# Kernel tuning notes

Measured on AMD Instinct MI355X. Metric: run time of the kernel, lower is better.

The kernel has to match this reference:

```python
import jax, jax.numpy as jnp
import numpy as np

D_MODEL = 1024
N_HEADS = 16
D_HEAD = D_MODEL // N_HEADS
B, S = 2, 2048


def setup_inputs() -> dict:
    key = jax.random.key(0)
    ks = jax.random.split(key, 14)
    std = 0.02
    inp = {
        "query": jax.random.normal(ks[0], (B, S, D_MODEL), dtype=jnp.float32),
        "key": jax.random.normal(ks[1], (B, S, D_MODEL), dtype=jnp.float32),
        "value": jax.random.normal(ks[2], (B, S, D_MODEL), dtype=jnp.float32),
        "mask": jax.random.randint(ks[3], (B, 1, S, S), 0, 2, dtype=jnp.int32),
        "position_bias": jax.random.normal(ks[4], (1, N_HEADS, S, S), dtype=jnp.float32),
        "w_q": jax.random.normal(ks[5], (D_MODEL, D_MODEL), dtype=jnp.float32) * std,
        "b_q": jnp.zeros((D_MODEL,), dtype=jnp.float32),
        "w_k": jax.random.normal(ks[6], (D_MODEL, D_MODEL), dtype=jnp.float32) * std,
        "b_k": jnp.zeros((D_MODEL,), dtype=jnp.float32),
        "w_v": jax.random.normal(ks[7], (D_MODEL, D_MODEL), dtype=jnp.float32) * std,
        "b_v": jnp.zeros((D_MODEL,), dtype=jnp.float32),
        "w_o": jax.random.normal(ks[8], (D_MODEL, D_MODEL), dtype=jnp.float32) * std,
        "b_o": jnp.zeros((D_MODEL,), dtype=jnp.float32),
    }
    return inp


def reference(query, key, value, mask, position_bias,
              w_q, b_q, w_k, b_k, w_v, b_v, w_o, b_o):
    b = query.shape[0]
    # projections: torch Linear computes x @ W^T + b
    def proj(x, w, bias):
        y = x @ w.T + bias                       # [b, s, D]
        return y.reshape(b, -1, N_HEADS, D_HEAD).transpose(0, 2, 1, 3)  # [b, h, s, d]

    Q = proj(query, w_q, b_q)
    K = proj(key, w_k, b_k)
    V = proj(value, w_v, b_v)

    scale = 1.0 / jnp.sqrt(jnp.asarray(D_HEAD, dtype=Q.dtype))
    scores = jnp.einsum("bhqd,bhkd->bhqk", Q, K) * scale
    scores = scores + position_bias
    scores = jnp.where(mask == 0, jnp.asarray(-1e9, dtype=scores.dtype), scores)
    attn = jax.nn.softmax(scores, axis=-1)       # dropout is identity at eval
    ctx = jnp.einsum("bhqk,bhkd->bhqd", attn, V)  # [b, h, s, d]
    ctx = ctx.transpose(0, 2, 1, 3).reshape(b, -1, N_HEADS * D_HEAD)
    return ctx @ w_o.T + b_o
```

## Files before the change

### kernel.cpp

```cpp
#include <hip/hip_runtime.h>
#include <hip/hip_bf16.h>

#define S_LEN 2048
#define DM 1024
#define NH 16
#define DH 64
#define MTOK 4096

typedef __attribute__((ext_vector_type(8))) __bf16 bf16x8;
typedef __attribute__((ext_vector_type(4))) float f32x4;
typedef unsigned short u16;
typedef unsigned long long u64;

__device__ __forceinline__ u16 f2bf(float f) {
  union { float f; unsigned u; } a; a.f = f;
  unsigned u = a.u;
  u += 0x7fffu + ((u >> 16) & 1u);
  return (u16)(u >> 16);
}

__device__ __forceinline__ bf16x8 ld_bf8(const u16* p) {
  return *reinterpret_cast<const bf16x8*>(p);
}

__device__ __forceinline__ float f4get(const float4& v, int r) {
  switch (r & 3) { case 0: return v.x; case 1: return v.y; case 2: return v.z; default: return v.w; }
}

__global__ void k_convert_all(
    const float* __restrict__ w_q, const float* __restrict__ w_k,
    const float* __restrict__ w_v, const float* __restrict__ w_o,
    const float* __restrict__ q, const float* __restrict__ k, const float* __restrict__ v,
    u16* __restrict__ dwq, u16* __restrict__ dwk, u16* __restrict__ dwv,
    u16* __restrict__ dwo, u16* __restrict__ dq, u16* __restrict__ dk, u16* __restrict__ dv,
    int n4w, int n4x) {
  const int z = blockIdx.y;
  const float* s; u16* d; int n4;
  switch (z) {
    case 0: s = w_q; d = dwq; n4 = n4w; break;
    case 1: s = w_k; d = dwk; n4 = n4w; break;
    case 2: s = w_v; d = dwv; n4 = n4w; break;
    case 3: s = w_o; d = dwo; n4 = n4w; break;
    case 4: s = q;   d = dq;  n4 = n4x; break;
    case 5: s = k;   d = dk;  n4 = n4x; break;
    default: s = v;  d = dv;  n4 = n4x; break;
  }
  int i = blockIdx.x * blockDim.x + threadIdx.x;
  const int stride = gridDim.x * blockDim.x;
  for (; i < n4; i += stride) {
    float4 vv = reinterpret_cast<const float4*>(s)[i];
    ushort4 o;
    o.x = f2bf(vv.x); o.y = f2bf(vv.y); o.z = f2bf(vv.z); o.w = f2bf(vv.w);
    reinterpret_cast<ushort4*>(d)[i] = o;
  }
}

__global__ void k_maskpack(const int* __restrict__ m, u64* __restrict__ o, int n) {
  int i = blockIdx.x * blockDim.x + threadIdx.x;
  int stride = gridDim.x * blockDim.x;
  for (; i < n; i += stride) {
    u64 bal = __ballot(m[i] != 0);
    if ((i & 63) == 0) o[i >> 6] = bal;
  }
}

__global__ __launch_bounds__(256) void k_gemm_qkv(
    const u16* __restrict__ xq, const u16* __restrict__ xk, const u16* __restrict__ xv,
    const u16* __restrict__ wq, const u16* __restrict__ wk, const u16* __restrict__ wv,
    const float* __restrict__ bq, const float* __restrict__ bk, const float* __restrict__ bvb,
    u16* __restrict__ Qd, u16* __restrict__ Kd, u16* __restrict__ Vd) {
  constexpr int K = DM;
  __shared__ u16 As[128 * 32];
  __shared__ u16 Bs[128 * 32];
  const int z = blockIdx.z;
  const u16* A  = z == 0 ? xq : z == 1 ? xk : xv;
  const u16* Bw = z == 0 ? wq : z == 1 ? wk : wv;
  const float* bias = z == 0 ? bq : z == 1 ? bk : bvb;
  const int tid = threadIdx.x;
  const int lane = tid & 63;
  const int wid = tid >> 6;
  const int wm = wid >> 1, wn = wid & 1;
  const int bm = blockIdx.x * 128;
  const int bn = blockIdx.y * 128;
  const int r0 = tid >> 2;
  const int c0 = (tid & 3) * 8;
  const int fr = lane & 15;
  const int fk = (lane >> 4) * 8;

  f32x4 acc[4][4] = {};

  const u16* ga = A + (size_t)(bm + r0) * K + c0;
  const u16* gb = Bw + (size_t)(bn + r0) * K + c0;

  for (int kt = 0; kt < K; kt += 32) {
    __syncthreads();
    __builtin_amdgcn_global_load_lds(
        (const __attribute__((address_space(1))) void*)(ga + kt),
        (__attribute__((address_space(3))) void*)(&As[r0 * 32 + c0]), 16, 0, 0);
    __builtin_amdgcn_global_load_lds(
        (const __attribute__((address_space(1))) void*)(ga + (size_t)64 * K + kt),
        (__attribute__((address_space(3))) void*)(&As[(r0 + 64) * 32 + c0]), 16, 0, 0);
    __builtin_amdgcn_global_load_lds(
        (const __attribute__((address_space(1))) void*)(gb + kt),
        (__attribute__((address_space(3))) void*)(&Bs[r0 * 32 + c0]), 16, 0, 0);
    __builtin_amdgcn_global_load_lds(
        (const __attribute__((address_space(1))) void*)(gb + (size_t)64 * K + kt),
        (__attribute__((address_space(3))) void*)(&Bs[(r0 + 64) * 32 + c0]), 16, 0, 0);
    __syncthreads();
    bf16x8 af[4], bfr[4];
#pragma unroll
    for (int m = 0; m < 4; ++m) af[m] = ld_bf8(&As[(wm * 64 + m * 16 + fr) * 32 + fk]);
#pragma unroll
    for (int n = 0; n < 4; ++n) bfr[n] = ld_bf8(&Bs[(wn * 64 + n * 16 + fr) * 32 + fk]);
#pragma unroll
    for (int m = 0; m < 4; ++m)
#pragma unroll
      for (int n = 0; n < 4; ++n)
        acc[m][n] = __builtin_amdgcn_mfma_f32_16x16x32_bf16(af[m], bfr[n], acc[m][n], 0, 0, 0);
  }

  const int cr = (lane >> 4) * 4;
  const int cc = lane & 15;
#pragma unroll
  for (int m = 0; m < 4; ++m) {
#pragma unroll
    for (int n = 0; n < 4; ++n) {
      const int colg = bn + wn * 64 + n * 16 + cc;
      const float bv = bias[colg];
      const int rbase = bm + wm * 64 + m * 16 + cr;
      const int hh = colg >> 6, d = colg & 63;
      if (z < 2) {
        u16* o = z == 0 ? Qd : Kd;
#pragma unroll
        for (int r = 0; r < 4; ++r) {
          const int tok = rbase + r;
          const int b = tok >> 11, s = tok & 2047;
          o[(((size_t)(b * NH + hh) * S_LEN) + s) * DH + d] = f2bf(acc[m][n][r] + bv);
        }
      } else {
        const int tok = rbase;
        const int b = tok >> 11, s = tok & 2047;
        ushort4 pk;
        pk.x = f2bf(acc[m][n][0] + bv);
        pk.y = f2bf(acc[m][n][1] + bv);
        pk.z = f2bf(acc[m][n][2] + bv);
        pk.w = f2bf(acc[m][n][3] + bv);
        *reinterpret_cast<ushort4*>(&Vd[(((size_t)(b * NH + hh) * DH) + d) * S_LEN + s]) = pk;
      }
    }
  }
}

__global__ __launch_bounds__(256) void k_gemm_out(
    const u16* __restrict__ A, const u16* __restrict__ Bw,
    const float* __restrict__ bias, float* __restrict__ dst) {
  constexpr int K = DM;
  __shared__ u16 As[128 * 32];
  __shared__ u16 Bs[128 * 32];
  const int tid = threadIdx.x;
  const int lane = tid & 63;
  const int wid = tid >> 6;
  const int wm = wid >> 1, wn = wid & 1;
  const int bm = blockIdx.x * 128;
  const int bn = blockIdx.y * 128;
  const int r0 = tid >> 2;
  const int c0 = (tid & 3) * 8;
  const int fr = lane & 15;
  const int fk = (lane >> 4) * 8;

  f32x4 acc[4][4] = {};

  const u16* ga = A + (size_t)(bm + r0) * K + c0;
  const u16* gb = Bw + (size_t)(bn + r0) * K + c0;

  for (int kt = 0; kt < K; kt += 32) {
    __syncthreads();
    __builtin_amdgcn_global_load_lds(
        (const __attribute__((address_space(1))) void*)(ga + kt),
        (__attribute__((address_space(3))) void*)(&As[r0 * 32 + c0]), 16, 0, 0);
    __builtin_amdgcn_global_load_lds(
        (const __attribute__((address_space(1))) void*)(ga + (size_t)64 * K + kt),
        (__attribute__((address_space(3))) void*)(&As[(r0 + 64) * 32 + c0]), 16, 0, 0);
    __builtin_amdgcn_global_load_lds(
        (const __attribute__((address_space(1))) void*)(gb + kt),
        (__attribute__((address_space(3))) void*)(&Bs[r0 * 32 + c0]), 16, 0, 0);
    __builtin_amdgcn_global_load_lds(
        (const __attribute__((address_space(1))) void*)(gb + (size_t)64 * K + kt),
        (__attribute__((address_space(3))) void*)(&Bs[(r0 + 64) * 32 + c0]), 16, 0, 0);
    __syncthreads();
    bf16x8 af[4], bfr[4];
#pragma unroll
    for (int m = 0; m < 4; ++m) af[m] = ld_bf8(&As[(wm * 64 + m * 16 + fr) * 32 + fk]);
#pragma unroll
    for (int n = 0; n < 4; ++n) bfr[n] = ld_bf8(&Bs[(wn * 64 + n * 16 + fr) * 32 + fk]);
#pragma unroll
    for (int m = 0; m < 4; ++m)
#pragma unroll
      for (int n = 0; n < 4; ++n)
        acc[m][n] = __builtin_amdgcn_mfma_f32_16x16x32_bf16(af[m], bfr[n], acc[m][n], 0, 0, 0);
  }

  const int cr = (lane >> 4) * 4;
  const int cc = lane & 15;
#pragma unroll
  for (int m = 0; m < 4; ++m) {
#pragma unroll
    for (int n = 0; n < 4; ++n) {
      const int colg = bn + wn * 64 + n * 16 + cc;
      const float bv = bias[colg];
      const int rbase = bm + wm * 64 + m * 16 + cr;
#pragma unroll
      for (int r = 0; r < 4; ++r)
        dst[(size_t)(rbase + r) * DM + colg] = acc[m][n][r] + bv;
    }
  }
}

__global__ __launch_bounds__(256, 4) void k_attn(
    const u16* __restrict__ Qb, const u16* __restrict__ Kb, const u16* __restrict__ Vt,
    const float* __restrict__ bias, const u64* __restrict__ mpk,
    u16* __restrict__ ctx) {
  __shared__ u16 lds[2][2][4096];
  const int tid = threadIdx.x;
  const int lane = tid & 63;
  const int w = tid >> 6;
  const int b = blockIdx.z;
  const int h = blockIdx.y;
  const int q0 = blockIdx.x * 64 + w * 16;
  const int lq = lane & 15;
  const int lg = lane >> 4;

  const float* bp = bias + (size_t)h * S_LEN * S_LEN;
  const u16* Kp = Kb + (size_t)(b * NH + h) * S_LEN * DH;
  const u16* Vp = Vt + (size_t)(b * NH + h) * DH * S_LEN;

  bf16x8 qf[2];
  f32x4 cacc[4] = {};
  float l_run = 0.f;
  {
    const u16* Qp = Qb + (size_t)(b * NH + h) * S_LEN * DH;
    qf[0] = ld_bf8(&Qp[(size_t)(q0 + lq) * DH + lg * 8]);
    qf[1] = ld_bf8(&Qp[(size_t)(q0 + lq) * DH + 32 + lg * 8]);
  }

#define STAGE(ktv, cb) {                                                          \
    _Pragma("unroll") for (int i = 0; i < 2; ++i) {                               \
      const int el = (i * 256 + tid) * 8;                                         \
      const int rr = el >> 6;                                                     \
      const int ce = ((tid & 7) * 8) ^ ((rr & 7) << 3);                           \
      const u16* ksrc = Kp + (size_t)((ktv) + rr) * DH + ce;                      \
      const u16* vsrc = Vp + (size_t)rr * S_LEN + (ktv) + ce;                     \
      __builtin_amdgcn_global_load_lds(                                           \
          (const __attribute__((address_space(1))) void*)ksrc,                    \
          (__attribute__((address_space(3))) void*)&lds[cb][0][el], 16, 0, 0);    \
      __builtin_amdgcn_global_load_lds(                                           \
          (const __attribute__((address_space(1))) void*)vsrc,                    \
          (__attribute__((address_space(3))) void*)&lds[cb][1][el], 16, 0, 0);    \
    } }

#define SWZ(row, col) ((row) * 64 + (((((col) >> 3) ^ ((row) & 7)) << 3) | ((col) & 7)))

#define LOADB(ktv, tv) {                                                          \
    bv0 = *reinterpret_cast<const float4*>(                                       \
        &bp[(size_t)(q0 + lq) * S_LEN + (ktv) + 0 * 16 + lg * 4]);                \
    bv1 = *reinterpret_cast<const float4*>(                                       \
        &bp[(size_t)(q0 + lq) * S_LEN + (ktv) + 1 * 16 + lg * 4]);                \
    bv2 = *reinterpret_cast<const float4*>(                                       \
        &bp[(size_t)(q0 + lq) * S_LEN + (ktv) + 2 * 16 + lg * 4]);                \
    bv3 = *reinterpret_cast<const float4*>(                                       \
        &bp[(size_t)(q0 + lq) * S_LEN + (ktv) + 3 * 16 + lg * 4]);                \
    mw = mpk[((size_t)(b * S_LEN + q0 + lq)) * 32 + (tv)]; }

  float4 bv0, bv1, bv2, bv3;
  u64 mw;
  STAGE(0, 0);
  LOADB(0, 0);
  int c = 0;
  for (int t = 0; t < S_LEN / 64; ++t) {
    __syncthreads();
    if (t + 1 < S_LEN / 64) STAGE(t * 64 + 64, c ^ 1);

    f32x4 sc[4];
    __builtin_amdgcn_s_setprio(1);
#pragma unroll
    for (int nb = 0; nb < 4; ++nb) {
      bf16x8 kf0 = ld_bf8(&lds[c][0][SWZ(nb * 16 + lq, lg * 8)]);
      bf16x8 kf1 = ld_bf8(&lds[c][0][SWZ(nb * 16 + lq, 32 + lg * 8)]);
      f32x4 z = {};
      z = __builtin_amdgcn_mfma_f32_16x16x32_bf16(kf0, qf[0], z, 0, 0, 0);
      sc[nb] = __builtin_amdgcn_mfma_f32_16x16x32_bf16(kf1, qf[1], z, 0, 0, 0);
    }
    __builtin_amdgcn_s_setprio(0);

#pragma unroll
    for (int r = 0; r < 4; ++r) {
      const int sh = lg * 4 + r;
      sc[0][r] = ((mw >> (sh))      & 1) ? sc[0][r] * 0.125f + f4get(bv0, r) : -1e9f;
      sc[1][r] = ((mw >> (16 + sh)) & 1) ? sc[1][r] * 0.125f + f4get(bv1, r) : -1e9f;
      sc[2][r] = ((mw >> (32 + sh)) & 1) ? sc[2][r] * 0.125f + f4get(bv2, r) : -1e9f;
      sc[3][r] = ((mw >> (48 + sh)) & 1) ? sc[3][r] * 0.125f + f4get(bv3, r) : -1e9f;
    }
    if (t + 1 < S_LEN / 64) LOADB(t * 64 + 64, t + 1);

    float s0 = 0.f;
#pragma unroll
    for (int nb = 0; nb < 4; ++nb)
#pragma unroll
      for (int r = 0; r < 4; ++r) {
        const float p = __expf(sc[nb][r]);
        sc[nb][r] = p;
        s0 += p;
      }
    s0 += __shfl_xor(s0, 16);
    s0 += __shfl_xor(s0, 32);
    l_run += s0;
    bf16x8 pa[2];
#pragma unroll
    for (int p = 0; p < 2; ++p) {
      union { __bf16 e[8]; bf16x8 v; } pu;
      pu.e[0] = (__bf16)sc[2 * p][0];     pu.e[1] = (__bf16)sc[2 * p][1];
      pu.e[2] = (__bf16)sc[2 * p][2];     pu.e[3] = (__bf16)sc[2 * p][3];
      pu.e[4] = (__bf16)sc[2 * p + 1][0]; pu.e[5] = (__bf16)sc[2 * p + 1][1];
      pu.e[6] = (__bf16)sc[2 * p + 1][2]; pu.e[7] = (__bf16)sc[2 * p + 1][3];
      pa[p] = pu.v;
    }
    __builtin_amdgcn_s_setprio(1);
#pragma unroll
    for (int nd = 0; nd < 4; ++nd) {
#pragma unroll
      for (int p = 0; p < 2; ++p) {
        union { unsigned u[4]; bf16x8 v; } vu;
        const unsigned* vp0 = reinterpret_cast<const unsigned*>(
            &lds[c][1][SWZ(nd * 16 + lq, (2 * p) * 16 + lg * 4)]);
        const unsigned* vp1 = reinterpret_cast<const unsigned*>(
            &lds[c][1][SWZ(nd * 16 + lq, (2 * p + 1) * 16 + lg * 4)]);
        vu.u[0] = vp0[0]; vu.u[1] = vp0[1];
        vu.u[2] = vp1[0]; vu.u[3] = vp1[1];
        cacc[nd] = __builtin_amdgcn_mfma_f32_16x16x32_bf16(pa[p], vu.v, cacc[nd], 0, 0, 0);
      }
    }
    __builtin_amdgcn_s_setprio(0);
    c ^= 1;
  }
#undef STAGE
#undef SWZ
#undef LOADB

#pragma unroll
  for (int r = 0; r < 4; ++r) {
    const float linv = 1.0f / __shfl(l_run, lg * 4 + r);
    const int tok = b * S_LEN + q0 + lg * 4 + r;
    u16* cp = ctx + (size_t)tok * DM + h * DH;
#pragma unroll
    for (int nd = 0; nd < 4; ++nd)
      cp[nd * 16 + lq] = f2bf(cacc[nd][r] * linv);
  }
}

extern "C" void kernel_launch(void* const* d_in, const int* in_sizes, int n_in,
                              void* d_out, int out_size, void* d_ws, size_t ws_size,
                              hipStream_t stream) {
  const float* q   = (const float*)d_in[0];
  const float* k   = (const float*)d_in[1];
  const float* v   = (const float*)d_in[2];
  const int*   msk = (const int*)d_in[3];
  const float* pb  = (const float*)d_in[4];
  const float* w_q = (const float*)d_in[5];
  const float* b_q = (const float*)d_in[6];
  const float* w_k = (const float*)d_in[7];
  const float* b_k = (const float*)d_in[8];
  const float* w_v = (const float*)d_in[9];
  const float* b_v = (const float*)d_in[10];
  const float* w_o = (const float*)d_in[11];
  const float* b_o = (const float*)d_in[12];
  float* out = (float*)d_out;

  char* ws = (char*)d_ws;
  u16* wq_bf = (u16*)(ws + ((size_t)0 << 20));
  u16* wk_bf = (u16*)(ws + ((size_t)2 << 20));
  u16* wv_bf = (u16*)(ws + ((size_t)4 << 20));
  u16* wo_bf = (u16*)(ws + ((size_t)6 << 20));
  u16* xq    = (u16*)(ws + ((size_t)8 << 20));
  u16* xk    = (u16*)(ws + ((size_t)16 << 20));
  u16* xv    = (u16*)(ws + ((size_t)24 << 20));
  u16* Qb    = (u16*)(ws + ((size_t)32 << 20));
  u16* Kb    = (u16*)(ws + ((size_t)40 << 20));
  u16* Vtb   = (u16*)(ws + ((size_t)48 << 20));
  u64* mpk   = (u64*)(ws + ((size_t)56 << 20));

  dim3 blk(256);
  const int n4w = DM * DM / 4;
  const int n4x = MTOK * DM / 4;

  k_convert_all<<<dim3(512, 7), blk, 0, stream>>>(
      w_q, w_k, w_v, w_o, q, k, v,
      wq_bf, wk_bf, wv_bf, wo_bf, xq, xk, xv, n4w, n4x);
  k_maskpack<<<dim3(2048), blk, 0, stream>>>(msk, mpk, 2 * S_LEN * S_LEN);

  k_gemm_qkv<<<dim3(32, 8, 3), blk, 0, stream>>>(
      xq, xk, xv, wq_bf, wk_bf, wv_bf, b_q, b_k, b_v, Qb, Kb, Vtb);

  k_attn<<<dim3(32, NH, 2), blk, 0, stream>>>(Qb, Kb, Vtb, pb, mpk, xq);
  k_gemm_out<<<dim3(32, 8), blk, 0, stream>>>(xq, wo_bf, b_o, out);
}
```

Baseline: 241.2 us.

## Software-pipeline PV of previous tile with QK of current tile using triple-buffered V

Restructures the attention loop so each iteration runs the P·V MFMAs for the previous key tile after computing the current tile's scores. V gets a third LDS buffer (K stays double-buffered) so the lagged P·V read does not race with the next stage's async loads. The full __syncthreads is replaced by an explicit vmcnt(5)/lgkmcnt(0) wait plus s_barrier, so only the K/V LDS loads must land while bias and mask loads stay in flight. LDS use rises from 32KB to 40KB per block, which may limit occupancy, and the hand-counted vmcnt assumes a fixed load issue order.

```diff
diff --git a/kernel.cpp b/kernel.cpp
--- a/kernel.cpp
+++ b/kernel.cpp
@@ -220,7 +220,7 @@
     const u16* __restrict__ Qb, const u16* __restrict__ Kb, const u16* __restrict__ Vt,
     const float* __restrict__ bias, const u64* __restrict__ mpk,
     u16* __restrict__ ctx) {
-  __shared__ u16 lds[2][2][4096];
+  __shared__ u16 lds[5 * 4096];
   const int tid = threadIdx.x;
   const int lane = tid & 63;
   const int w = tid >> 6;
@@ -243,7 +243,7 @@
     qf[1] = ld_bf8(&Qp[(size_t)(q0 + lq) * DH + 32 + lg * 8]);
   }
 
-#define STAGE(ktv, cb) {                                                          \
+#define STAGE(ktv, KOFF, VOFF) {                                                  \
     _Pragma("unroll") for (int i = 0; i < 2; ++i) {                               \
       const int el = (i * 256 + tid) * 8;                                         \
       const int rr = el >> 6;                                                     \
@@ -252,10 +252,10 @@
       const u16* vsrc = Vp + (size_t)rr * S_LEN + (ktv) + ce;                     \
       __builtin_amdgcn_global_load_lds(                                           \
           (const __attribute__((address_space(1))) void*)ksrc,                    \
-          (__attribute__((address_space(3))) void*)&lds[cb][0][el], 16, 0, 0);    \
+          (__attribute__((address_space(3))) void*)&lds[(KOFF) + el], 16, 0, 0);  \
       __builtin_amdgcn_global_load_lds(                                           \
           (const __attribute__((address_space(1))) void*)vsrc,                    \
-          (__attribute__((address_space(3))) void*)&lds[cb][1][el], 16, 0, 0);    \
+          (__attribute__((address_space(3))) void*)&lds[(VOFF) + el], 16, 0, 0);  \
     } }
 
 #define SWZ(row, col) ((row) * 64 + (((((col) >> 3) ^ ((row) & 7)) << 3) | ((col) & 7)))
@@ -271,21 +271,51 @@
         &bp[(size_t)(q0 + lq) * S_LEN + (ktv) + 3 * 16 + lg * 4]);                \
     mw = mpk[((size_t)(b * S_LEN + q0 + lq)) * 32 + (tv)]; }
 
+#define PVSTEP(VOFF, PA0, PA1) {                                                  \
+    __builtin_amdgcn_s_setprio(1);                                                \
+    _Pragma("unroll") for (int nd = 0; nd < 4; ++nd) {                            \
+      _Pragma("unroll") for (int p = 0; p < 2; ++p) {                             \
+        union { unsigned u[4]; bf16x8 v; } vu;                                    \
+        const unsigned* vp0 = reinterpret_cast<const unsigned*>(                  \
+            &lds[(VOFF) + SWZ(nd * 16 + lq, (2 * p) * 16 + lg * 4)]);             \
+        const unsigned* vp1 = reinterpret_cast<const unsigned*>(                  \
+            &lds[(VOFF) + SWZ(nd * 16 + lq, (2 * p + 1) * 16 + lg * 4)]);         \
+        vu.u[0] = vp0[0]; vu.u[1] = vp0[1];                                       \
+        vu.u[2] = vp1[0]; vu.u[3] = vp1[1];                                       \
+        cacc[nd] = __builtin_amdgcn_mfma_f32_16x16x32_bf16(p ? PA1 : PA0, vu.v,   \
+                                                           cacc[nd], 0, 0, 0);    \
+      }                                                                           \
+    }                                                                             \
+    __builtin_amdgcn_s_setprio(0); }
+
   float4 bv0, bv1, bv2, bv3;
   u64 mw;
-  STAGE(0, 0);
+  bf16x8 paA0, paA1, paB0, paB1;
+  int kc = 0;
+  int vprv = 4 * 4096;
+  int vcur = 2 * 4096;
+  int vstg = 3 * 4096;
+
+  STAGE(0, kc, vcur);
   LOADB(0, 0);
-  int c = 0;
+
   for (int t = 0; t < S_LEN / 64; ++t) {
-    __syncthreads();
-    if (t + 1 < S_LEN / 64) STAGE(t * 64 + 64, c ^ 1);
+    asm volatile("s_waitcnt vmcnt(5) lgkmcnt(0)" ::: "memory");
+    __builtin_amdgcn_sched_barrier(0);
+    __builtin_amdgcn_s_barrier();
+    __builtin_amdgcn_sched_barrier(0);
+
+    if (t + 1 < S_LEN / 64) {
+      STAGE(t * 64 + 64, kc ^ 4096, vstg);
+      __builtin_amdgcn_sched_barrier(0);
+    }
 
     f32x4 sc[4];
     __builtin_amdgcn_s_setprio(1);
 #pragma unroll
     for (int nb = 0; nb < 4; ++nb) {
-      bf16x8 kf0 = ld_bf8(&lds[c][0][SWZ(nb * 16 + lq, lg * 8)]);
-      bf16x8 kf1 = ld_bf8(&lds[c][0][SWZ(nb * 16 + lq, 32 + lg * 8)]);
+      bf16x8 kf0 = ld_bf8(&lds[kc + SWZ(nb * 16 + lq, lg * 8)]);
+      bf16x8 kf1 = ld_bf8(&lds[kc + SWZ(nb * 16 + lq, 32 + lg * 8)]);
       f32x4 z = {};
       z = __builtin_amdgcn_mfma_f32_16x16x32_bf16(kf0, qf[0], z, 0, 0, 0);
       sc[nb] = __builtin_amdgcn_mfma_f32_16x16x32_bf16(kf1, qf[1], z, 0, 0, 0);
@@ -314,37 +344,32 @@
     s0 += __shfl_xor(s0, 16);
     s0 += __shfl_xor(s0, 32);
     l_run += s0;
-    bf16x8 pa[2];
-#pragma unroll
-    for (int p = 0; p < 2; ++p) {
+
+    if (t > 0) PVSTEP(vprv, paA0, paA1);
+
+    {
       union { __bf16 e[8]; bf16x8 v; } pu;
-      pu.e[0] = (__bf16)sc[2 * p][0];     pu.e[1] = (__bf16)sc[2 * p][1];
-      pu.e[2] = (__bf16)sc[2 * p][2];     pu.e[3] = (__bf16)sc[2 * p][3];
-      pu.e[4] = (__bf16)sc[2 * p + 1][0]; pu.e[5] = (__bf16)sc[2 * p + 1][1];
-      pu.e[6] = (__bf16)sc[2 * p + 1][2]; pu.e[7] = (__bf16)sc[2 * p + 1][3];
-      pa[p] = pu.v;
-    }
-    __builtin_amdgcn_s_setprio(1);
-#pragma unroll
-    for (int nd = 0; nd < 4; ++nd) {
-#pragma unroll
-      for (int p = 0; p < 2; ++p) {
-        union { unsigned u[4]; bf16x8 v; } vu;
-        const unsigned* vp0 = reinterpret_cast<const unsigned*>(
-            &lds[c][1][SWZ(nd * 16 + lq, (2 * p) * 16 + lg * 4)]);
-        const unsigned* vp1 = reinterpret_cast<const unsigned*>(
-            &lds[c][1][SWZ(nd * 16 + lq, (2 * p + 1) * 16 + lg * 4)]);
-        vu.u[0] = vp0[0]; vu.u[1] = vp0[1];
-        vu.u[2] = vp1[0]; vu.u[3] = vp1[1];
-        cacc[nd] = __builtin_amdgcn_mfma_f32_16x16x32_bf16(pa[p], vu.v, cacc[nd], 0, 0, 0);
-      }
-    }
-    __builtin_amdgcn_s_setprio(0);
-    c ^= 1;
-  }
+      pu.e[0] = (__bf16)sc[0][0]; pu.e[1] = (__bf16)sc[0][1];
+      pu.e[2] = (__bf16)sc[0][2]; pu.e[3] = (__bf16)sc[0][3];
+      pu.e[4] = (__bf16)sc[1][0]; pu.e[5] = (__bf16)sc[1][1];
+      pu.e[6] = (__bf16)sc[1][2]; pu.e[7] = (__bf16)sc[1][3];
+      paB0 = pu.v;
+      pu.e[0] = (__bf16)sc[2][0]; pu.e[1] = (__bf16)sc[2][1];
+      pu.e[2] = (__bf16)sc[2][2]; pu.e[3] = (__bf16)sc[2][3];
+      pu.e[4] = (__bf16)sc[3][0]; pu.e[5] = (__bf16)sc[3][1];
+      pu.e[6] = (__bf16)sc[3][2]; pu.e[7] = (__bf16)sc[3][3];
+      paB1 = pu.v;
+    }
+    paA0 = paB0; paA1 = paB1;
+
+    kc ^= 4096;
+    const int vtmp = vprv; vprv = vcur; vcur = vstg; vstg = vtmp;
+  }
+  PVSTEP(vprv, paA0, paA1);
 #undef STAGE
 #undef SWZ
 #undef LOADB
+#undef PVSTEP
 
 #pragma unroll
   for (int r = 0; r < 4; ++r) {
```

New measurement: 303.5 us. +25.9%, slower.
